# Performance work log

Hardware: AMD Instinct MI355X
Metric: run time of the kernel (lower is better)

## Reference

```python
import jax, jax.numpy as jnp
import numpy as np

SIZE_SUBMAP = 1024          # points per submap (module global in repo)
RATIO = 0.5                 # CONFIG['Detector']['ratio']
K_POS = int(SIZE_SUBMAP * RATIO)  # 512
K = 32                      # self.k, fps ratio = K / K_POS
B = 2048                    # number of submaps in batch


def fps_single(pts, k):
    """Deterministic farthest point sampling (start at index 0). pts: [n,3] -> [k] int indices."""
    min_d = jnp.sum((pts - pts[0]) ** 2, axis=-1)  # [n]

    def step(min_d, _):
        idx = jnp.argmax(min_d)
        d2 = jnp.sum((pts - pts[idx]) ** 2, axis=-1)
        return jnp.minimum(min_d, d2), idx

    _, idxs = jax.lax.scan(step, min_d, None, length=k - 1)
    return jnp.concatenate([jnp.zeros((1,), dtype=idxs.dtype), idxs])


def setup_inputs() -> dict:
    key = jax.random.key(0)
    ks = jax.random.split(key, 8)
    n = B * SIZE_SUBMAP
    x = jax.random.normal(ks[0], (n, 32), jnp.float32)
    pos = jax.random.normal(ks[1], (n, 3), jnp.float32) * 10.0
    batch = jnp.repeat(jnp.arange(B, dtype=jnp.int32), SIZE_SUBMAP)
    # MLP([32,16,8]) -> Linear(8,1) -> Softplus
    W1 = jax.random.normal(ks[2], (32, 16), jnp.float32) / np.sqrt(32.0)
    b1 = jnp.zeros((16,), jnp.float32)
    W2 = jax.random.normal(ks[3], (16, 8), jnp.float32) / np.sqrt(16.0)
    b2 = jnp.zeros((8,), jnp.float32)
    W3 = jax.random.normal(ks[4], (8, 1), jnp.float32) / np.sqrt(8.0)
    b3 = jnp.zeros((1,), jnp.float32)
    return {"x": x, "pos": pos, "batch": batch,
            "W1": W1, "b1": b1, "W2": W2, "b2": b2, "W3": W3, "b3": b3}


def reference(x, pos, batch, W1, b1, W2, b2, W3, b3):
    bsz = batch.shape[0] // SIZE_SUBMAP  # static batch_size (= batch.max()+1)
    # small per-point MLP + Softplus score
    h = jax.nn.relu(x @ W1 + b1)
    h = jax.nn.relu(h @ W2 + b2)
    s = jax.nn.softplus(h @ W3 + b3)          # [B*N, 1]
    x_batch = s.reshape(bsz, -1)               # [B, N]
    pos_b = pos.reshape(bsz, -1, 3)            # [B, N, 3]
    # distance of xy-coords to submap center
    dist = jnp.linalg.norm(pos_b[..., :2], axis=-1)     # [B, N]
    # k_pos closest points (topk of -dist)
    _, idx1 = jax.lax.top_k(-dist, K_POS)               # [B, K_POS]
    pos_sel = jnp.take_along_axis(pos_b, idx1[..., None], axis=1)  # [B, K_POS, 3]
    # batched farthest point sampling, K points per submap (within-batch indices)
    key_idx = jax.vmap(lambda p: fps_single(p, K))(pos_sel)        # [B, K]
    original_indices = jnp.take_along_axis(idx1, key_idx, axis=1)  # [B, K]
    weights = jnp.take_along_axis(x_batch, original_indices, axis=1)  # [B, K]
    return weights, original_indices
```

## Files before the change

kernel.cpp:

```cpp
#include <hip/hip_runtime.h>
#include <math.h>
#include <stdint.h>

#define N_PTS 1024
#define K_POS 512
#define K_FPS 32

typedef unsigned long long u64;
typedef unsigned int u32;

__device__ __forceinline__ u64 shfl_xor_u64(u64 v, int mask) {
    return __shfl_xor(v, mask, 64);
}

__device__ __forceinline__ void shuffle_stage(u64 key[16], int j, int k, int lane) {
    #pragma unroll
    for (int r = 0; r < 16; ++r) {
        int e = (r << 6) | lane;
        u64 o = shfl_xor_u64(key[r], j);
        bool up      = ((e & k) == 0);
        bool lowhalf = ((lane & j) == 0);
        bool keep = ((key[r] < o) == (lowhalf == up));
        key[r] = keep ? key[r] : o;
    }
}

template<int JR, int KR>
__device__ __forceinline__ void intra_stage(u64 key[16]) {
    #pragma unroll
    for (int r = 0; r < 16; ++r) {
        if ((r & JR) == 0) {
            const int r2 = r | JR;
            const bool up = ((r & KR) == 0);
            u64 a = key[r], c = key[r2];
            u64 lo = (a < c) ? a : c;
            u64 hi = (a < c) ? c : a;
            key[r]  = up ? lo : hi;
            key[r2] = up ? hi : lo;
        }
    }
}

__global__ __launch_bounds__(256) void sortfps_kernel(
    const float* __restrict__ pos,
    float* __restrict__ out_idx,
    int B)
{
#pragma clang fp contract(off)
    const int lane = threadIdx.x & 63;
    const int b    = blockIdx.x * 4 + (threadIdx.x >> 6);
    if (b >= B) return;

    const float* pb = pos + (size_t)b * N_PTS * 3;

    u64 key[16];
    #pragma unroll
    for (int r = 0; r < 16; ++r) {
        int e = (r << 6) | lane;
        float x = pb[e * 3 + 0];
        float y = pb[e * 3 + 1];
        float xx = x * x, yy = y * y;
        float d = sqrtf(xx + yy);
        key[r] = ((u64)__float_as_uint(d) << 32) | (u32)e;
    }

    for (int k = 2; k <= 64; k <<= 1)
        for (int j = k >> 1; j > 0; j >>= 1)
            shuffle_stage(key, j, k, lane);
    intra_stage<1, 2>(key);
    for (int j = 32; j > 0; j >>= 1) shuffle_stage(key, j, 128, lane);
    intra_stage<2, 4>(key);
    intra_stage<1, 4>(key);
    for (int j = 32; j > 0; j >>= 1) shuffle_stage(key, j, 256, lane);
    intra_stage<4, 8>(key);
    intra_stage<2, 8>(key);
    intra_stage<1, 8>(key);
    for (int j = 32; j > 0; j >>= 1) shuffle_stage(key, j, 512, lane);
    intra_stage<8, 16>(key);
    intra_stage<4, 16>(key);
    intra_stage<2, 16>(key);
    intra_stage<1, 16>(key);
    for (int j = 32; j > 0; j >>= 1) shuffle_stage(key, j, 1024, lane);


    float px[8], py[8], pz[8], pidx[8], mind[8];
    #pragma unroll
    for (int r = 0; r < 8; ++r) {
        int orig = (int)(u32)(key[r] & 0xffffffffu);
        px[r] = pb[orig * 3 + 0];
        py[r] = pb[orig * 3 + 1];
        pz[r] = pb[orig * 3 + 2];
        pidx[r] = (float)orig;
    }

    float wx = __shfl(px[0], 0, 64);
    float wy = __shfl(py[0], 0, 64);
    float wz = __shfl(pz[0], 0, 64);
    float wi = __shfl(pidx[0], 0, 64);

    float* ob = out_idx + (size_t)b * K_FPS;
    if (lane == 0) ob[0] = wi;

    #pragma unroll
    for (int r = 0; r < 8; ++r) {
        float dx = px[r] - wx, dy = py[r] - wy, dz = pz[r] - wz;
        float u0 = dx * dx, u1 = dy * dy, u2 = dz * dz;
        mind[r] = (u0 + u1) + u2;
    }

    for (int it = 1; it < K_FPS; ++it) {
        u64 best = 0;
        #pragma unroll
        for (int r = 0; r < 8; ++r) {
            int e = r * 64 + lane;
            u64 kk = ((u64)__float_as_uint(mind[r]) << 32) |
                     (u64)(0xffffffffu - (u32)e);
            if (kk > best) best = kk;
        }
        #pragma unroll
        for (int off = 32; off > 0; off >>= 1) {
            u64 o = shfl_xor_u64(best, off);
            if (o > best) best = o;
        }
        int ew = (int)(0xffffffffu - (u32)(best & 0xffffffffu));
        int rw = ew >> 6, lw = ew & 63;
        float sx = 0.f, sy = 0.f, sz = 0.f, si = 0.f;
        #pragma unroll
        for (int r = 0; r < 8; ++r)
            if (r == rw) { sx = px[r]; sy = py[r]; sz = pz[r]; si = pidx[r]; }
        wx = __shfl(sx, lw, 64);
        wy = __shfl(sy, lw, 64);
        wz = __shfl(sz, lw, 64);
        wi = __shfl(si, lw, 64);
        if (lane == 0) ob[it] = wi;

        #pragma unroll
        for (int r = 0; r < 8; ++r) {
            float dx = px[r] - wx, dy = py[r] - wy, dz = pz[r] - wz;
            float u0 = dx * dx, u1 = dy * dy, u2 = dz * dz;
            float d2 = (u0 + u1) + u2;
            mind[r] = fminf(mind[r], d2);
        }
    }
}

__global__ __launch_bounds__(256) void mlp_kernel(
    const float* __restrict__ x,
    const float* __restrict__ W1, const float* __restrict__ b1,
    const float* __restrict__ W2, const float* __restrict__ b2,
    const float* __restrict__ W3, const float* __restrict__ b3,
    const float* __restrict__ idx_f,
    float* __restrict__ out_w, int total)
{
    __shared__ float sW1[32 * 16];
    __shared__ float sW2[16 * 8];
    __shared__ float sW3[8];
    __shared__ float sb1[16];
    __shared__ float sb2[8];
    __shared__ float sb3;

    for (int i = threadIdx.x; i < 512; i += 256) sW1[i] = W1[i];
    if (threadIdx.x < 128) sW2[threadIdx.x] = W2[threadIdx.x];
    if (threadIdx.x < 16)  sb1[threadIdx.x] = b1[threadIdx.x];
    if (threadIdx.x < 8) {
        sb2[threadIdx.x] = b2[threadIdx.x];
        sW3[threadIdx.x] = W3[threadIdx.x];
    }
    if (threadIdx.x == 0) sb3 = b3[0];
    __syncthreads();

    int t = blockIdx.x * 256 + threadIdx.x;
    if (t >= total) return;

    int b    = t >> 5;
    int orig = (int)(idx_f[t] + 0.5f);
    const float* xr = x + ((size_t)b * N_PTS + (size_t)orig) * 32;

    float xi[32];
    #pragma unroll
    for (int i = 0; i < 32; i += 4) {
        float4 v = *(const float4*)(xr + i);
        xi[i] = v.x; xi[i + 1] = v.y; xi[i + 2] = v.z; xi[i + 3] = v.w;
    }

    float h1[16];
    #pragma unroll
    for (int j = 0; j < 16; ++j) {
        float a = sb1[j];
        #pragma unroll
        for (int i = 0; i < 32; ++i) a += xi[i] * sW1[i * 16 + j];
        h1[j] = fmaxf(a, 0.0f);
    }
    float h2[8];
    #pragma unroll
    for (int j = 0; j < 8; ++j) {
        float a = sb2[j];
        #pragma unroll
        for (int i = 0; i < 16; ++i) a += h1[i] * sW2[i * 8 + j];
        h2[j] = fmaxf(a, 0.0f);
    }
    float v = sb3;
    #pragma unroll
    for (int i = 0; i < 8; ++i) v += h2[i] * sW3[i];

    float sp = fmaxf(v, 0.0f) + log1pf(expf(-fabsf(v)));
    out_w[t] = sp;
}

extern "C" void kernel_launch(void* const* d_in, const int* in_sizes, int n_in,
                              void* d_out, int out_size, void* d_ws, size_t ws_size,
                              hipStream_t stream) {
    const float* x   = (const float*)d_in[0];
    const float* pos = (const float*)d_in[1];
    const float* W1 = (const float*)d_in[3];
    const float* b1 = (const float*)d_in[4];
    const float* W2 = (const float*)d_in[5];
    const float* b2 = (const float*)d_in[6];
    const float* W3 = (const float*)d_in[7];
    const float* b3 = (const float*)d_in[8];

    const int B = in_sizes[2] / N_PTS;
    float* out_w = (float*)d_out;
    float* out_i = (float*)d_out + (size_t)B * K_FPS;

    sortfps_kernel<<<(B + 3) / 4, 256, 0, stream>>>(pos, out_i, B);

    const int total = B * K_FPS;
    mlp_kernel<<<(total + 255) / 256, 256, 0, stream>>>(
        x, W1, b1, W2, b2, W3, b3, out_i, out_w, total);
}
```

Measured before the change: 392.8 us.

## Use blocked lane-major bitonic sort layout, stage points in LDS, simplify FPS argmax

Switches the bitonic sort to a blocked layout where each lane owns 16 consecutive points, so the first ten stages and the low strides of every later stage run in registers and only the high strides need cross-lane shuffles. Point coordinates are loaded once as vectorized float4 reads, written to shared memory, and gathered from there for FPS instead of from global memory. The FPS loop tracks the per-lane best point directly, reduces over 32 lanes with int shuffles, then uses ballot and readlane to pick the winner. Risks include higher register pressure from 16-wide arrays and 48 KB of shared memory per block, which may limit occupancy; tie-breaking changes from lowest element index to lowest lane then lowest register.

After: 386.6 us. No clear change (-1.6%).

```diff
diff --git a/kernel.cpp b/kernel.cpp
--- a/kernel.cpp
+++ b/kernel.cpp
@@ -13,31 +13,32 @@
     return __shfl_xor(v, mask, 64);
 }
 
-__device__ __forceinline__ void shuffle_stage(u64 key[16], int j, int k, int lane) {
-    #pragma unroll
-    for (int r = 0; r < 16; ++r) {
-        int e = (r << 6) | lane;
-        u64 o = shfl_xor_u64(key[r], j);
-        bool up      = ((e & k) == 0);
-        bool lowhalf = ((lane & j) == 0);
-        bool keep = ((key[r] < o) == (lowhalf == up));
-        key[r] = keep ? key[r] : o;
-    }
-}
-
-template<int JR, int KR>
-__device__ __forceinline__ void intra_stage(u64 key[16]) {
-    #pragma unroll
-    for (int r = 0; r < 16; ++r) {
-        if ((r & JR) == 0) {
-            const int r2 = r | JR;
-            const bool up = ((r & KR) == 0);
+template<int J>
+__device__ __forceinline__ void intra_stage(u64 key[16], int lane, int k) {
+    #pragma unroll
+    for (int r = 0; r < 16; ++r) {
+        if ((r & J) == 0) {
+            const int r2 = r | J;
+            int p = (lane << 4) | r;
+            bool up = ((p & k) == 0);
             u64 a = key[r], c = key[r2];
-            u64 lo = (a < c) ? a : c;
-            u64 hi = (a < c) ? c : a;
+            bool sw = a < c;
+            u64 lo = sw ? a : c;
+            u64 hi = sw ? c : a;
             key[r]  = up ? lo : hi;
             key[r2] = up ? hi : lo;
         }
+    }
+}
+
+__device__ __forceinline__ void cross_stage(u64 key[16], int lane, int m, int k) {
+    bool low = ((lane & m) == 0);
+    bool up  = ((lane & (k >> 4)) == 0);
+    bool sel = (low == up);
+    #pragma unroll
+    for (int r = 0; r < 16; ++r) {
+        u64 o = shfl_xor_u64(key[r], m);
+        key[r] = ((key[r] < o) == sel) ? key[r] : o;
     }
 }
 
@@ -48,94 +49,113 @@
 {
 #pragma clang fp contract(off)
     const int lane = threadIdx.x & 63;
-    const int b    = blockIdx.x * 4 + (threadIdx.x >> 6);
+    const int sub  = threadIdx.x >> 6;
+    const int b    = blockIdx.x * 4 + sub;
+
+    __shared__ float spts[4][N_PTS * 3];
+
     if (b >= B) return;
 
     const float* pb = pos + (size_t)b * N_PTS * 3;
 
+    float4 f4[12];
+    {
+        const float4* pb4 = (const float4*)pb + (size_t)lane * 12;
+        #pragma unroll
+        for (int i = 0; i < 12; ++i) f4[i] = pb4[i];
+        float4* sp4 = (float4*)&spts[sub][0] + lane * 12;
+        #pragma unroll
+        for (int i = 0; i < 12; ++i) sp4[i] = f4[i];
+    }
+    const float* f = (const float*)&f4[0];
+
     u64 key[16];
     #pragma unroll
     for (int r = 0; r < 16; ++r) {
-        int e = (r << 6) | lane;
-        float x = pb[e * 3 + 0];
-        float y = pb[e * 3 + 1];
+        int p = (lane << 4) | r;
+        float x = f[r * 3 + 0];
+        float y = f[r * 3 + 1];
         float xx = x * x, yy = y * y;
         float d = sqrtf(xx + yy);
-        key[r] = ((u64)__float_as_uint(d) << 32) | (u32)e;
-    }
-
-    for (int k = 2; k <= 64; k <<= 1)
-        for (int j = k >> 1; j > 0; j >>= 1)
-            shuffle_stage(key, j, k, lane);
-    intra_stage<1, 2>(key);
-    for (int j = 32; j > 0; j >>= 1) shuffle_stage(key, j, 128, lane);
-    intra_stage<2, 4>(key);
-    intra_stage<1, 4>(key);
-    for (int j = 32; j > 0; j >>= 1) shuffle_stage(key, j, 256, lane);
-    intra_stage<4, 8>(key);
-    intra_stage<2, 8>(key);
-    intra_stage<1, 8>(key);
-    for (int j = 32; j > 0; j >>= 1) shuffle_stage(key, j, 512, lane);
-    intra_stage<8, 16>(key);
-    intra_stage<4, 16>(key);
-    intra_stage<2, 16>(key);
-    intra_stage<1, 16>(key);
-    for (int j = 32; j > 0; j >>= 1) shuffle_stage(key, j, 1024, lane);
-
-
-    float px[8], py[8], pz[8], pidx[8], mind[8];
-    #pragma unroll
-    for (int r = 0; r < 8; ++r) {
+        key[r] = ((u64)__float_as_uint(d) << 32) | (u32)p;
+    }
+
+    intra_stage<1>(key, lane, 2);
+    intra_stage<2>(key, lane, 4);
+    intra_stage<1>(key, lane, 4);
+    intra_stage<4>(key, lane, 8);
+    intra_stage<2>(key, lane, 8);
+    intra_stage<1>(key, lane, 8);
+    intra_stage<8>(key, lane, 16);
+    intra_stage<4>(key, lane, 16);
+    intra_stage<2>(key, lane, 16);
+    intra_stage<1>(key, lane, 16);
+    #pragma unroll 1
+    for (int k = 32; k <= N_PTS; k <<= 1) {
+        #pragma unroll 1
+        for (int j = k >> 1; j >= 16; j >>= 1)
+            cross_stage(key, lane, j >> 4, k);
+        intra_stage<8>(key, lane, k);
+        intra_stage<4>(key, lane, k);
+        intra_stage<2>(key, lane, k);
+        intra_stage<1>(key, lane, k);
+    }
+
+
+    float px[16], py[16], pz[16], pidx[16], mind[16];
+    #pragma unroll
+    for (int r = 0; r < 16; ++r) {
         int orig = (int)(u32)(key[r] & 0xffffffffu);
-        px[r] = pb[orig * 3 + 0];
-        py[r] = pb[orig * 3 + 1];
-        pz[r] = pb[orig * 3 + 2];
+        const float* sp = &spts[sub][orig * 3];
+        px[r] = sp[0]; py[r] = sp[1]; pz[r] = sp[2];
         pidx[r] = (float)orig;
     }
 
-    float wx = __shfl(px[0], 0, 64);
-    float wy = __shfl(py[0], 0, 64);
-    float wz = __shfl(pz[0], 0, 64);
-    float wi = __shfl(pidx[0], 0, 64);
-
     float* ob = out_idx + (size_t)b * K_FPS;
-    if (lane == 0) ob[0] = wi;
-
-    #pragma unroll
-    for (int r = 0; r < 8; ++r) {
+    float wx = __uint_as_float(__builtin_amdgcn_readlane(__float_as_uint(px[0]), 0));
+    float wy = __uint_as_float(__builtin_amdgcn_readlane(__float_as_uint(py[0]), 0));
+    float wz = __uint_as_float(__builtin_amdgcn_readlane(__float_as_uint(pz[0]), 0));
+    if (lane == 0) ob[0] = pidx[0];
+
+    #pragma unroll
+    for (int r = 0; r < 16; ++r) {
         float dx = px[r] - wx, dy = py[r] - wy, dz = pz[r] - wz;
         float u0 = dx * dx, u1 = dy * dy, u2 = dz * dz;
         mind[r] = (u0 + u1) + u2;
     }
+    if (lane >= 32) {
+        #pragma unroll
+        for (int r = 0; r < 16; ++r) mind[r] = -INFINITY;
+    }
 
     for (int it = 1; it < K_FPS; ++it) {
-        u64 best = 0;
-        #pragma unroll
-        for (int r = 0; r < 8; ++r) {
-            int e = r * 64 + lane;
-            u64 kk = ((u64)__float_as_uint(mind[r]) << 32) |
-                     (u64)(0xffffffffu - (u32)e);
-            if (kk > best) best = kk;
-        }
-        #pragma unroll
-        for (int off = 32; off > 0; off >>= 1) {
-            u64 o = shfl_xor_u64(best, off);
-            if (o > best) best = o;
-        }
-        int ew = (int)(0xffffffffu - (u32)(best & 0xffffffffu));
-        int rw = ew >> 6, lw = ew & 63;
-        float sx = 0.f, sy = 0.f, sz = 0.f, si = 0.f;
-        #pragma unroll
-        for (int r = 0; r < 8; ++r)
-            if (r == rw) { sx = px[r]; sy = py[r]; sz = pz[r]; si = pidx[r]; }
-        wx = __shfl(sx, lw, 64);
-        wy = __shfl(sy, lw, 64);
-        wz = __shfl(sz, lw, 64);
-        wi = __shfl(si, lw, 64);
+        float bv = mind[0], bx = px[0], by = py[0], bz = pz[0], bi = pidx[0];
+        #pragma unroll
+        for (int r = 1; r < 16; ++r) {
+            bool g = mind[r] > bv;
+            bv = g ? mind[r] : bv;
+            bx = g ? px[r] : bx;
+            by = g ? py[r] : by;
+            bz = g ? pz[r] : bz;
+            bi = g ? pidx[r] : bi;
+        }
+        int bvi = __float_as_int(bv);
+        int g = bvi;
+        #pragma unroll
+        for (int m = 1; m <= 16; m <<= 1) {
+            int o = __shfl_xor(g, m, 64);
+            g = (o > g) ? o : g;
+        }
+        u64 mask = __ballot(bvi == g) & 0xffffffffull;
+        int W = __ffsll((unsigned long long)mask) - 1;
+        wx = __uint_as_float(__builtin_amdgcn_readlane(__float_as_uint(bx), W));
+        wy = __uint_as_float(__builtin_amdgcn_readlane(__float_as_uint(by), W));
+        wz = __uint_as_float(__builtin_amdgcn_readlane(__float_as_uint(bz), W));
+        float wi = __uint_as_float(__builtin_amdgcn_readlane(__float_as_uint(bi), W));
         if (lane == 0) ob[it] = wi;
 
         #pragma unroll
-        for (int r = 0; r < 8; ++r) {
+        for (int r = 0; r < 16; ++r) {
             float dx = px[r] - wx, dy = py[r] - wy, dz = pz[r] - wz;
             float u0 = dx * dx, u1 = dy * dy, u2 = dz * dz;
             float d2 = (u0 + u1) + u2;
```
